# Kernel optimization log

Measured on AMD Instinct MI355X. Metric: run time of the kernel, lower is better.

The kernel has to match this reference:

```python
import jax, jax.numpy as jnp
import numpy as np

G = 128          # voxel grid extent per axis
KS = 3           # kernel size per axis
KK = KS ** 3     # 27 kernel offsets
N_IN, N_OUT, C_IN, C_OUT = 50000, 100000, 128, 128


def setup_inputs() -> dict:
    key = jax.random.key(0)
    k1, k2, k3, k4 = jax.random.split(key, 4)
    features = jax.random.normal(k1, (N_IN, C_IN), dtype=jnp.float32)
    W = jax.random.normal(k2, (KK, C_IN, C_OUT), dtype=jnp.float32) * (1.0 / np.sqrt(C_IN * KK))
    inp_positions = jax.random.randint(k3, (N_IN, 3), 0, G, dtype=jnp.int32)
    out_positions = jax.random.randint(k4, (N_OUT, 3), 0, G, dtype=jnp.int32)
    return {"features": features, "W": W,
            "inp_positions": inp_positions, "out_positions": out_positions}


def _kernel_offsets():
    r = np.arange(KS) - KS // 2  # [-1, 0, 1] for KS=3 (offset=0 since KS is odd)
    dx, dy, dz = np.meshgrid(r, r, r, indexing="ij")
    return jnp.asarray(np.stack([dx.ravel(), dy.ravel(), dz.ravel()], axis=1), dtype=jnp.int32)  # [KK,3]


def reference(features, W, inp_positions, out_positions):
    # Sparse conv-transpose: voxelize input points (voxel_size=1, offset=0 -> identity
    # on integer coords), build voxel->input-index hash (dense grid table), then for
    # each output point gather the input feature at each of the KK kernel offsets and
    # accumulate W[k'] @ feat with mirrored kernel index (transpose of SparseConv).
    lin_in = (inp_positions[:, 0] * G + inp_positions[:, 1]) * G + inp_positions[:, 2]
    grid = jnp.full((G * G * G,), -1, dtype=jnp.int32)
    grid = grid.at[lin_in].max(jnp.arange(N_IN, dtype=jnp.int32))  # deterministic on dup voxels

    offsets = _kernel_offsets()          # [KK, 3]
    W_mirror = W[::-1]                   # transpose conv uses mirrored kernel index

    def step(acc, xk):
        off, Wk = xk                     # off [3], Wk [C_IN, C_OUT]
        nb = out_positions + off[None, :]               # [N_OUT, 3]
        in_bounds = jnp.all((nb >= 0) & (nb < G), axis=1)
        lin = (nb[:, 0] * G + nb[:, 1]) * G + nb[:, 2]
        idx = grid[jnp.clip(lin, 0, G * G * G - 1)]      # [N_OUT]
        ok = in_bounds & (idx >= 0)
        f = jnp.where(ok[:, None], features[jnp.clip(idx, 0)], 0.0)  # [N_OUT, C_IN]
        return acc + f @ Wk, None

    acc0 = jnp.zeros((out_positions.shape[0], W.shape[2]), dtype=features.dtype)
    out, _ = jax.lax.scan(step, acc0, (offsets, W_mirror))
    return out
```

## Files before the change

### kernel.cpp

```cpp
#include <hip/hip_runtime.h>
#include <hip/hip_bf16.h>

#define G    128
#define GGG  (G * G * G)
#define C    128
#define KK   27
#define CAP  4096
#define RT   16

typedef __attribute__((ext_vector_type(8))) short bf16x8;
typedef __attribute__((ext_vector_type(4))) float f32x4;

__device__ __forceinline__ ushort f2b(float f) {
    __hip_bfloat16 h = __float2bfloat16(f);
    return *reinterpret_cast<ushort*>(&h);
}

#define WT_BLOCKS 108
__global__ __launch_bounds__(256) void prep5_kernel(
    uint4* __restrict__ grid16_4, int* __restrict__ cnt,
    const float* __restrict__ W, ushort* __restrict__ Wtb,
    const float4* __restrict__ fg4, uint2* __restrict__ fb2, int nf4)
{
    if (blockIdx.x < WT_BLOCKS) {
        int mm = blockIdx.x >> 2;
        int t  = blockIdx.x & 3;
        __shared__ float Ls[32][129];
        const float* src = W + (size_t)mm * C * C + (size_t)(t * 32) * C;
#pragma unroll
        for (int k = 0; k < 16; ++k) {
            int q = threadIdx.x + k * 256;
            int r = q >> 7, co = q & 127;
            Ls[r][co] = src[r * C + co];
        }
        __syncthreads();
        ushort* dst = Wtb + (size_t)(KK - 1 - mm) * C * C + t * 32;
#pragma unroll
        for (int k = 0; k < 4; ++k) {
            int q = threadIdx.x + k * 256;
            int co = q >> 3, j = q & 7;
            union { ushort u[4]; uint2 p; } pk;
            pk.u[0] = f2b(Ls[4*j+0][co]);
            pk.u[1] = f2b(Ls[4*j+1][co]);
            pk.u[2] = f2b(Ls[4*j+2][co]);
            pk.u[3] = f2b(Ls[4*j+3][co]);
            *(uint2*)&dst[co * C + 4 * j] = pk.p;
        }
        return;
    }
    int b = blockIdx.x - WT_BLOCKS;
    int nb = gridDim.x - WT_BLOCKS;
    int tid = b * 256 + threadIdx.x;
    int stride = nb * 256;
    uint4 ffff = {0xFFFFFFFFu, 0xFFFFFFFFu, 0xFFFFFFFFu, 0xFFFFFFFFu};
    for (int i = tid; i < GGG * 2 / 16; i += stride) grid16_4[i] = ffff;
    if (tid < KK) cnt[tid] = 0;
    for (int i = tid; i < nf4; i += stride) {
        float4 v = fg4[i];
        union { ushort u[4]; uint2 p; } pk;
        pk.u[0] = f2b(v.x); pk.u[1] = f2b(v.y);
        pk.u[2] = f2b(v.z); pk.u[3] = f2b(v.w);
        fb2[i] = pk.p;
    }
}

__global__ void scatter16_kernel(const int* __restrict__ pos,
                                 unsigned int* __restrict__ gword, int n) {
    int i = blockIdx.x * blockDim.x + threadIdx.x;
    if (i >= n) return;
    int x = pos[3 * i], y = pos[3 * i + 1], z = pos[3 * i + 2];
    int lin = (x * G + y) * G + z;
    unsigned int* w = &gword[lin >> 1];
    int sh = (lin & 1) * 16;
    unsigned int val = (unsigned int)i;
    unsigned int old = *w, assumed;
    do {
        unsigned int cur = (old >> sh) & 0xFFFFu;
        if (cur != 0xFFFFu && cur >= val) break;
        unsigned int nw = (old & ~(0xFFFFu << sh)) | (val << sh);
        assumed = old;
        old = atomicCAS(w, assumed, nw);
    } while (old != assumed);
}

__global__ __launch_bounds__(256) void compact4_kernel(
    const int* __restrict__ out_pos, const ushort* __restrict__ grid16,
    int* __restrict__ cnt, int2* __restrict__ pairs,
    int* __restrict__ cnt_row, int* __restrict__ rowtap, int n_out)
{
    int row = blockIdx.x * 256 + threadIdx.x;
    bool valid = row < n_out;
    int lane = threadIdx.x & 63;

    int px = 0, py = 0, pz = 0;
    if (valid) { px = out_pos[3*row]; py = out_pos[3*row+1]; pz = out_pos[3*row+2]; }

    int idx[KK];
#pragma unroll
    for (int m = 0; m < KK; ++m) {
        int x = px + m / 9 - 1, y = py + (m % 9) / 3 - 1, z = pz + m % 3 - 1;
        bool inb = valid && (unsigned)x < G && (unsigned)y < G && (unsigned)z < G;
        int v = inb ? (int)grid16[(x * G + y) * G + z] : 0xFFFF;
        idx[m] = (v == 0xFFFF) ? -1 : v;
    }

    __shared__ int bcnt[KK], bbase[KK];
    if (threadIdx.x < KK) bcnt[threadIdx.x] = 0;
    __syncthreads();

    int gl[KK];
#pragma unroll
    for (int m = 0; m < KK; ++m) {
        unsigned long long act = __ballot(idx[m] >= 0);
        int lpre = __popcll(act & ((1ull << lane) - 1ull));
        int wcnt = __popcll(act);
        int wbase = 0;
        if (lane == 0 && wcnt) wbase = atomicAdd(&bcnt[m], wcnt);
        wbase = __shfl(wbase, 0);
        gl[m] = wbase + lpre;
    }
    __syncthreads();
    if (threadIdx.x < KK) bbase[threadIdx.x] = atomicAdd(&cnt[threadIdx.x], bcnt[threadIdx.x]);
    __syncthreads();

    int gs[KK];
    int cr = 0;
#pragma unroll
    for (int m = 0; m < KK; ++m) {
        int g = -1;
        if (idx[m] >= 0) {
            g = bbase[m] + gl[m];
            if (g >= CAP) g = -1;
        }
        gs[m] = g;
        if (g >= 0) ++cr;
    }

    int dest = (cr == 1) ? row : -1;
    int k = 0;
#pragma unroll
    for (int m = 0; m < KK; ++m) {
        int g = gs[m];
        if (g >= 0) {
            pairs[m * CAP + g] = make_int2(idx[m], dest);
            if (k < RT) { rowtap[k * n_out + row] = (g << 5) | m; ++k; }
        }
    }
    if (valid) cnt_row[row] = cr;
}

__global__ __launch_bounds__(256, 2) void pair_mm5_kernel(
    const uint4* __restrict__ featb4, const ushort* __restrict__ Wtb,
    const int2* __restrict__ pairs, const int* __restrict__ cnt,
    ushort* __restrict__ part, float* __restrict__ out)
{
    int m = blockIdx.y;
    int nm = min(cnt[m], CAP);
    if ((int)(blockIdx.x * 128) >= nm) return;

    __shared__ ushort Wl[128 * 136];
    __shared__ ushort Af[128 * 136];
    __shared__ int    idx_s[128];
    __shared__ int    dest_s[128];

    {
        const uint4* src = (const uint4*)(Wtb + (size_t)m * C * C);
        uint4* dst = (uint4*)Wl;
        for (int q = threadIdx.x; q < 2048; q += 256) {
            int r = q >> 4, c = q & 15;
            dst[r * 17 + c] = src[q];
        }
    }

    int lane = threadIdx.x & 63;
    int w    = threadIdx.x >> 6;
    int l15  = lane & 15;
    int quad = lane >> 4;
    uint4* Af4 = (uint4*)Af;

    for (int base = blockIdx.x * 128; base < nm; base += gridDim.x * 128) {
        __syncthreads();
        if (threadIdx.x < 128) {
            int g = base + threadIdx.x;
            int2 pr = (g < nm) ? pairs[m * CAP + g] : make_int2(-1, -1);
            idx_s[threadIdx.x]  = pr.x;
            dest_s[threadIdx.x] = pr.y;
        }
        __syncthreads();

#pragma unroll
        for (int k = 0; k < 8; ++k) {
            int q = threadIdx.x + k * 256;
            int r = q >> 4, c = q & 15;
            int id = idx_s[r];
            if (id >= 0) Af4[r * 17 + c] = featb4[(size_t)id * 16 + c];
        }
        __syncthreads();

        f32x4 acc[2][8];
#pragma unroll
        for (int s = 0; s < 2; ++s)
#pragma unroll
            for (int n = 0; n < 8; ++n) acc[s][n] = (f32x4){0.f, 0.f, 0.f, 0.f};

#pragma unroll
        for (int kk = 0; kk < 4; ++kk) {
            bf16x8 a0 = *(bf16x8*)&Af[(32*w + l15)      * 136 + kk * 32 + quad * 8];
            bf16x8 a1 = *(bf16x8*)&Af[(32*w + 16 + l15) * 136 + kk * 32 + quad * 8];
#pragma unroll
            for (int n = 0; n < 8; ++n) {
                bf16x8 b = *(bf16x8*)&Wl[(n * 16 + l15) * 136 + kk * 32 + quad * 8];
                acc[0][n] = __builtin_amdgcn_mfma_f32_16x16x32_bf16(a0, b, acc[0][n], 0, 0, 0);
                acc[1][n] = __builtin_amdgcn_mfma_f32_16x16x32_bf16(a1, b, acc[1][n], 0, 0, 0);
            }
        }

#pragma unroll
        for (int s = 0; s < 2; ++s) {
            int r0 = 32 * w + 16 * s + quad * 4;
#pragma unroll
            for (int reg = 0; reg < 4; ++reg) {
                int r = r0 + reg;
                if (base + r >= nm) continue;
                int d = dest_s[r];
                if (d >= 0) {
                    float* o = out + (size_t)d * C + l15;
#pragma unroll
                    for (int n = 0; n < 8; ++n) o[n * 16] = acc[s][n][reg];
                } else {
                    ushort* p = part + ((size_t)(m * CAP + base + r)) * C + l15;
#pragma unroll
                    for (int n = 0; n < 8; ++n) p[n * 16] = f2b(acc[s][n][reg]);
                }
            }
        }
    }
}

__global__ __launch_bounds__(256) void gather_sum3_kernel(
    const ushort* __restrict__ part, const int* __restrict__ rowtap,
    const int* __restrict__ cnt_row, float* __restrict__ out, int n_out)
{
    int row0 = blockIdx.x * 16;
    int rl = threadIdx.x >> 4;
    int t  = threadIdx.x & 15;
    int row = row0 + rl;

    __shared__ int rt_s[RT][16];
    __shared__ int cnt_s[16];
    __shared__ int maxc;
    if (threadIdx.x < 16) {
        int r = row0 + threadIdx.x;
        cnt_s[threadIdx.x] = (r < n_out) ? cnt_row[r] : 0;
    }
    __syncthreads();
    if (threadIdx.x == 0) {
        int mx = 0;
#pragma unroll
        for (int i = 0; i < 16; ++i) mx = max(mx, cnt_s[i]);
        maxc = mx;
    }
    __syncthreads();
    {
        int k = threadIdx.x >> 4, r = threadIdx.x & 15;
        if (k < maxc)
            rt_s[k][r] = (row0 + r < n_out) ? rowtap[k * n_out + row0 + r] : 0;
    }
    __syncthreads();

    int nt = cnt_s[rl];
    if (nt == 1) return;

    float acc[8] = {0,0,0,0,0,0,0,0};
    for (int k = 0; k < nt; ++k) {
        int e = rt_s[k][rl];
        int m = e & 31, g = e >> 5;
        uint4 v = *(const uint4*)(part + ((size_t)(m * CAP + g)) * C + t * 8);
        acc[0] += __uint_as_float(v.x << 16);
        acc[1] += __uint_as_float(v.x & 0xffff0000u);
        acc[2] += __uint_as_float(v.y << 16);
        acc[3] += __uint_as_float(v.y & 0xffff0000u);
        acc[4] += __uint_as_float(v.z << 16);
        acc[5] += __uint_as_float(v.z & 0xffff0000u);
        acc[6] += __uint_as_float(v.w << 16);
        acc[7] += __uint_as_float(v.w & 0xffff0000u);
    }
    if (row < n_out) {
        float* o = out + (size_t)row * C + t * 8;
        *(float4*)(o)     = (float4){acc[0], acc[1], acc[2], acc[3]};
        *(float4*)(o + 4) = (float4){acc[4], acc[5], acc[6], acc[7]};
    }
}

__global__ void init2_kernel(int4* __restrict__ grid4, int* __restrict__ cnt) {
    int i = blockIdx.x * blockDim.x + threadIdx.x;
    int stride = gridDim.x * blockDim.x;
    int4 mone = {-1, -1, -1, -1};
    for (int j = i; j < GGG / 4; j += stride) grid4[j] = mone;
    if (i < KK) cnt[i] = 0;
}

__global__ void scatter_kernel(const int* __restrict__ pos,
                               int* __restrict__ grid, int n) {
    int i = blockIdx.x * blockDim.x + threadIdx.x;
    if (i >= n) return;
    int x = pos[3 * i], y = pos[3 * i + 1], z = pos[3 * i + 2];
    atomicMax(&grid[(x * G + y) * G + z], i);
}

__global__ __launch_bounds__(128) void gather_mm_kernel(
    const float* __restrict__ features, const float* __restrict__ W,
    const int* __restrict__ out_pos, const int* __restrict__ grid,
    float* __restrict__ out, int n_out)
{
    int row = blockIdx.x;
    if (row >= n_out) return;
    int c = threadIdx.x;
    __shared__ int   nb_idx[KK];
    __shared__ float feat_s[C];
    int px = out_pos[3*row], py = out_pos[3*row+1], pz = out_pos[3*row+2];
    if (c < KK) {
        int i = c / 9, j = (c % 9) / 3, k = c % 3;
        int x = px + i - 1, y = py + j - 1, z = pz + k - 1;
        int idx = -1;
        if ((unsigned)x < G && (unsigned)y < G && (unsigned)z < G)
            idx = grid[(x * G + y) * G + z];
        nb_idx[c] = idx;
    }
    __syncthreads();
    float acc = 0.f;
    for (int m = 0; m < KK; ++m) {
        int idx = nb_idx[m];
        if (idx < 0) continue;
        __syncthreads();
        feat_s[c] = features[idx * C + c];
        __syncthreads();
        const float* __restrict__ Wk = W + (KK - 1 - m) * C * C + c;
        float a = 0.f;
#pragma unroll
        for (int ci = 0; ci < C; ++ci) a += feat_s[ci] * Wk[ci * C];
        acc += a;
    }
    out[row * C + c] = acc;
}

extern "C" void kernel_launch(void* const* d_in, const int* in_sizes, int n_in,
                              void* d_out, int out_size, void* d_ws, size_t ws_size,
                              hipStream_t stream) {
    const float* features = (const float*)d_in[0];
    const float* W        = (const float*)d_in[1];
    const int*   inp_pos  = (const int*)d_in[2];
    const int*   out_pos  = (const int*)d_in[3];
    float*       out      = (float*)d_out;

    int n_in_pts  = in_sizes[2] / 3;
    int n_out_pts = out_size / C;

    size_t o_grid   = 0;
    size_t o_cnt    = (size_t)GGG * 4;
    size_t o_pairs  = (o_cnt + 256 + 255) & ~(size_t)255;
    size_t o_cntr   = (o_pairs + (size_t)KK * CAP * 8 + 255) & ~(size_t)255;
    size_t o_rowtap = (o_cntr + (size_t)n_out_pts * 4 + 255) & ~(size_t)255;
    size_t o_wtb    = (o_rowtap + (size_t)RT * n_out_pts * 4 + 255) & ~(size_t)255;
    size_t o_featb  = (o_wtb + (size_t)KK * C * C * 2 + 255) & ~(size_t)255;
    size_t o_part   = (o_featb + (size_t)n_in_pts * C * 2 + 255) & ~(size_t)255;
    size_t need     = o_part + (size_t)KK * CAP * C * 2;

    ushort* grid16  = (ushort*)((char*)d_ws + o_grid);
    int*    cnt     = (int*)((char*)d_ws + o_cnt);
    int2*   pairs   = (int2*)((char*)d_ws + o_pairs);
    int*    cnt_row = (int*)((char*)d_ws + o_cntr);
    int*    rowtap  = (int*)((char*)d_ws + o_rowtap);
    ushort* Wtb     = (ushort*)((char*)d_ws + o_wtb);
    ushort* featb   = (ushort*)((char*)d_ws + o_featb);
    ushort* part    = (ushort*)((char*)d_ws + o_part);

    if (ws_size < need) {
        int* grid32 = (int*)d_ws;
        hipLaunchKernelGGL(init2_kernel, dim3(2048), dim3(256), 0, stream,
                           (int4*)grid32, cnt);
        hipLaunchKernelGGL(scatter_kernel, dim3((n_in_pts + 255) / 256), dim3(256), 0, stream,
                           inp_pos, grid32, n_in_pts);
        hipLaunchKernelGGL(gather_mm_kernel, dim3(n_out_pts), dim3(128), 0, stream,
                           features, W, out_pos, grid32, out, n_out_pts);
        return;
    }

    hipLaunchKernelGGL(prep5_kernel, dim3(WT_BLOCKS + 916), dim3(256), 0, stream,
                       (uint4*)grid16, cnt, W, Wtb,
                       (const float4*)features, (uint2*)featb, n_in_pts * C / 4);
    hipLaunchKernelGGL(scatter16_kernel, dim3((n_in_pts + 255) / 256), dim3(256), 0, stream,
                       inp_pos, (unsigned int*)grid16, n_in_pts);
    hipLaunchKernelGGL(compact4_kernel, dim3((n_out_pts + 255) / 256), dim3(256), 0, stream,
                       out_pos, grid16, cnt, pairs, cnt_row, rowtap, n_out_pts);
    hipLaunchKernelGGL(pair_mm5_kernel, dim3(19, KK), dim3(256), 0, stream,
                       (const uint4*)featb, Wtb, pairs, cnt, part, out);
    hipLaunchKernelGGL(gather_sum3_kernel, dim3((n_out_pts + 15) / 16), dim3(256), 0, stream,
                       part, rowtap, cnt_row, out, n_out_pts);
}
```

Measured before the change: 135.3 us.

## Fuse all conv stages into one cooperative persistent kernel with grid syncs

Replaces the five-kernel pipeline with a single cooperative kernel of 512 persistent blocks that runs prep, scatter, compaction, MFMA pair matmul and gather-sum, separated by grid-wide barriers. It also goes back from a 16-bit packed voxel grid with CAS loops to a 32-bit grid using atomicMax. The aim is to remove launch gaps and inter-kernel drain between stages. In exchange it adds grid-sync overhead, doubles the grid clear and lookup traffic, and limits parallelism to a fixed block count. A multi-kernel fallback is kept for when cooperative launch fails.

```diff
diff --git a/kernel.cpp b/kernel.cpp
--- a/kernel.cpp
+++ b/kernel.cpp
@@ -1,5 +1,8 @@
 #include <hip/hip_runtime.h>
 #include <hip/hip_bf16.h>
+#include <hip/hip_cooperative_groups.h>
+
+namespace cg = cooperative_groups;
 
 #define G    128
 #define GGG  (G * G * G)
@@ -7,6 +10,8 @@
 #define KK   27
 #define CAP  4096
 #define RT   16
+#define NBLK 512
+#define NTHR 256
 
 typedef __attribute__((ext_vector_type(8))) short bf16x8;
 typedef __attribute__((ext_vector_type(4))) float f32x4;
@@ -16,98 +21,326 @@
     return *reinterpret_cast<ushort*>(&h);
 }
 
-#define WT_BLOCKS 108
-__global__ __launch_bounds__(256) void prep5_kernel(
-    uint4* __restrict__ grid16_4, int* __restrict__ cnt,
-    const float* __restrict__ W, ushort* __restrict__ Wtb,
-    const float4* __restrict__ fg4, uint2* __restrict__ fb2, int nf4)
+struct SmemA { float Ls[32][129]; };
+struct SmemB { int bcnt[KK]; int bbase[KK]; };
+struct SmemC { ushort Wl[128 * 136]; ushort Af[128 * 136]; int idx[128]; int dest[128]; };
+struct SmemD { int rt[RT][16]; int cnt[16]; int maxc; };
+union SmemU { SmemA a; SmemB b; SmemC c; SmemD d; };
+
+__global__ __launch_bounds__(NTHR, 2) void fused_kernel(
+    const float* __restrict__ features, const float* __restrict__ W,
+    const int* __restrict__ inp_pos, const int* __restrict__ out_pos,
+    float* __restrict__ out, int* __restrict__ grid32, int* __restrict__ cnt,
+    int2* __restrict__ pairs, int* __restrict__ cnt_row, int* __restrict__ rowtap,
+    ushort* __restrict__ Wtb, ushort* __restrict__ featb, ushort* __restrict__ part,
+    int n_in, int n_out)
 {
-    if (blockIdx.x < WT_BLOCKS) {
-        int mm = blockIdx.x >> 2;
-        int t  = blockIdx.x & 3;
-        __shared__ float Ls[32][129];
-        const float* src = W + (size_t)mm * C * C + (size_t)(t * 32) * C;
-#pragma unroll
-        for (int k = 0; k < 16; ++k) {
-            int q = threadIdx.x + k * 256;
-            int r = q >> 7, co = q & 127;
-            Ls[r][co] = src[r * C + co];
-        }
-        __syncthreads();
-        ushort* dst = Wtb + (size_t)(KK - 1 - mm) * C * C + t * 32;
-#pragma unroll
-        for (int k = 0; k < 4; ++k) {
-            int q = threadIdx.x + k * 256;
-            int co = q >> 3, j = q & 7;
+    cg::grid_group gg = cg::this_grid();
+    __shared__ SmemU sm;
+    int tid = blockIdx.x * NTHR + threadIdx.x;
+    const int gstride = NBLK * NTHR;
+    int lane = threadIdx.x & 63;
+
+    {
+        int4* g4 = (int4*)grid32;
+        int4 mone = {-1, -1, -1, -1};
+        for (int i = tid; i < GGG / 4; i += gstride) g4[i] = mone;
+        if (tid < 32) cnt[tid] = 0;
+
+        const float4* f4 = (const float4*)features;
+        uint2* fb2 = (uint2*)featb;
+        int nf4 = n_in * C / 4;
+        for (int i = tid; i < nf4; i += gstride) {
+            float4 v = f4[i];
             union { ushort u[4]; uint2 p; } pk;
-            pk.u[0] = f2b(Ls[4*j+0][co]);
-            pk.u[1] = f2b(Ls[4*j+1][co]);
-            pk.u[2] = f2b(Ls[4*j+2][co]);
-            pk.u[3] = f2b(Ls[4*j+3][co]);
-            *(uint2*)&dst[co * C + 4 * j] = pk.p;
-        }
-        return;
-    }
-    int b = blockIdx.x - WT_BLOCKS;
-    int nb = gridDim.x - WT_BLOCKS;
-    int tid = b * 256 + threadIdx.x;
-    int stride = nb * 256;
-    uint4 ffff = {0xFFFFFFFFu, 0xFFFFFFFFu, 0xFFFFFFFFu, 0xFFFFFFFFu};
-    for (int i = tid; i < GGG * 2 / 16; i += stride) grid16_4[i] = ffff;
-    if (tid < KK) cnt[tid] = 0;
+            pk.u[0] = f2b(v.x); pk.u[1] = f2b(v.y);
+            pk.u[2] = f2b(v.z); pk.u[3] = f2b(v.w);
+            fb2[i] = pk.p;
+        }
+
+        if (blockIdx.x < KK * 4) {
+            int mm = blockIdx.x >> 2;
+            int t  = blockIdx.x & 3;
+            const float* src = W + (size_t)mm * C * C + (size_t)(t * 32) * C;
+#pragma unroll
+            for (int k = 0; k < 16; ++k) {
+                int q = threadIdx.x + k * 256;
+                int r = q >> 7, co = q & 127;
+                sm.a.Ls[r][co] = src[r * C + co];
+            }
+            __syncthreads();
+            ushort* dst = Wtb + (size_t)(KK - 1 - mm) * C * C + t * 32;
+#pragma unroll
+            for (int k = 0; k < 4; ++k) {
+                int q = threadIdx.x + k * 256;
+                int co = q >> 3, j = q & 7;
+                union { ushort u[4]; uint2 p; } pk;
+                pk.u[0] = f2b(sm.a.Ls[4*j+0][co]);
+                pk.u[1] = f2b(sm.a.Ls[4*j+1][co]);
+                pk.u[2] = f2b(sm.a.Ls[4*j+2][co]);
+                pk.u[3] = f2b(sm.a.Ls[4*j+3][co]);
+                *(uint2*)&dst[co * C + 4 * j] = pk.p;
+            }
+        }
+    }
+    gg.sync();
+
+    for (int i = tid; i < n_in; i += gstride) {
+        int x = inp_pos[3 * i], y = inp_pos[3 * i + 1], z = inp_pos[3 * i + 2];
+        atomicMax(&grid32[(x * G + y) * G + z], i);
+    }
+    gg.sync();
+
+    int nchunk = (n_out + NTHR - 1) / NTHR;
+    for (int ch = blockIdx.x; ch < nchunk; ch += NBLK) {
+        __syncthreads();
+        int row = ch * NTHR + threadIdx.x;
+        bool valid = row < n_out;
+        int px = 0, py = 0, pz = 0;
+        if (valid) { px = out_pos[3*row]; py = out_pos[3*row+1]; pz = out_pos[3*row+2]; }
+
+        int idx[KK];
+#pragma unroll
+        for (int m = 0; m < KK; ++m) {
+            int x = px + m / 9 - 1, y = py + (m % 9) / 3 - 1, z = pz + m % 3 - 1;
+            bool inb = valid && (unsigned)x < G && (unsigned)y < G && (unsigned)z < G;
+            idx[m] = inb ? grid32[(x * G + y) * G + z] : -1;
+        }
+
+        if (threadIdx.x < KK) sm.b.bcnt[threadIdx.x] = 0;
+        __syncthreads();
+
+        int gl[KK];
+#pragma unroll
+        for (int m = 0; m < KK; ++m) {
+            unsigned long long act = __ballot(idx[m] >= 0);
+            int lpre = __popcll(act & ((1ull << lane) - 1ull));
+            int wcnt = __popcll(act);
+            int wbase = 0;
+            if (lane == 0 && wcnt) wbase = atomicAdd(&sm.b.bcnt[m], wcnt);
+            wbase = __shfl(wbase, 0);
+            gl[m] = wbase + lpre;
+        }
+        __syncthreads();
+        if (threadIdx.x < KK)
+            sm.b.bbase[threadIdx.x] = atomicAdd(&cnt[threadIdx.x], sm.b.bcnt[threadIdx.x]);
+        __syncthreads();
+
+        int gs[KK];
+        int cr = 0;
+#pragma unroll
+        for (int m = 0; m < KK; ++m) {
+            int g = -1;
+            if (idx[m] >= 0) {
+                g = sm.b.bbase[m] + gl[m];
+                if (g >= CAP) g = -1;
+            }
+            gs[m] = g;
+            if (g >= 0) ++cr;
+        }
+
+        int dest = (cr == 1) ? row : -1;
+        int k = 0;
+#pragma unroll
+        for (int m = 0; m < KK; ++m) {
+            int g = gs[m];
+            if (g >= 0) {
+                pairs[m * CAP + g] = make_int2(idx[m], dest);
+                if (k < RT) { rowtap[k * n_out + row] = (g << 5) | m; ++k; }
+            }
+        }
+        if (valid) cnt_row[row] = cr;
+    }
+    gg.sync();
+
+    {
+        int w    = threadIdx.x >> 6;
+        int l15  = lane & 15;
+        int quad = lane >> 4;
+        const uint4* featb4 = (const uint4*)featb;
+        uint4* Af4 = (uint4*)sm.c.Af;
+        const int ntile = KK * (CAP / 128);
+
+        for (int t = blockIdx.x; t < ntile; t += NBLK) {
+            int m = t >> 5;
+            int base = (t & 31) * 128;
+            int nm = min(cnt[m], CAP);
+            if (base >= nm) continue;
+
+            __syncthreads();
+            {
+                const uint4* src = (const uint4*)(Wtb + (size_t)m * C * C);
+                uint4* dst = (uint4*)sm.c.Wl;
+                for (int q = threadIdx.x; q < 2048; q += 256) {
+                    int r = q >> 4, c = q & 15;
+                    dst[r * 17 + c] = src[q];
+                }
+            }
+            if (threadIdx.x < 128) {
+                int g = base + threadIdx.x;
+                int2 pr = (g < nm) ? pairs[m * CAP + g] : make_int2(-1, -1);
+                sm.c.idx[threadIdx.x]  = pr.x;
+                sm.c.dest[threadIdx.x] = pr.y;
+            }
+            __syncthreads();
+
+#pragma unroll
+            for (int k = 0; k < 8; ++k) {
+                int q = threadIdx.x + k * 256;
+                int r = q >> 4, c = q & 15;
+                int id = sm.c.idx[r];
+                if (id >= 0) Af4[r * 17 + c] = featb4[(size_t)id * 16 + c];
+            }
+            __syncthreads();
+
+            f32x4 acc[2][8];
+#pragma unroll
+            for (int s = 0; s < 2; ++s)
+#pragma unroll
+                for (int n = 0; n < 8; ++n) acc[s][n] = (f32x4){0.f, 0.f, 0.f, 0.f};
+
+#pragma unroll
+            for (int kk = 0; kk < 4; ++kk) {
+                bf16x8 a0 = *(bf16x8*)&sm.c.Af[(32*w + l15)      * 136 + kk * 32 + quad * 8];
+                bf16x8 a1 = *(bf16x8*)&sm.c.Af[(32*w + 16 + l15) * 136 + kk * 32 + quad * 8];
+#pragma unroll
+                for (int n = 0; n < 8; ++n) {
+                    bf16x8 b = *(bf16x8*)&sm.c.Wl[(n * 16 + l15) * 136 + kk * 32 + quad * 8];
+                    acc[0][n] = __builtin_amdgcn_mfma_f32_16x16x32_bf16(a0, b, acc[0][n], 0, 0, 0);
+                    acc[1][n] = __builtin_amdgcn_mfma_f32_16x16x32_bf16(a1, b, acc[1][n], 0, 0, 0);
+                }
+            }
+
+#pragma unroll
+            for (int s = 0; s < 2; ++s) {
+                int r0 = 32 * w + 16 * s + quad * 4;
+#pragma unroll
+                for (int reg = 0; reg < 4; ++reg) {
+                    int r = r0 + reg;
+                    if (base + r >= nm) continue;
+                    int d = sm.c.dest[r];
+                    if (d >= 0) {
+                        float* o = out + (size_t)d * C + l15;
+#pragma unroll
+                        for (int n = 0; n < 8; ++n) o[n * 16] = acc[s][n][reg];
+                    } else {
+                        ushort* p = part + ((size_t)(m * CAP + base + r)) * C + l15;
+#pragma unroll
+                        for (int n = 0; n < 8; ++n) p[n * 16] = f2b(acc[s][n][reg]);
+                    }
+                }
+            }
+        }
+    }
+    gg.sync();
+
+    {
+        int rl = threadIdx.x >> 4;
+        int t16 = threadIdx.x & 15;
+        int ngrp = (n_out + 15) / 16;
+        for (int gi = blockIdx.x; gi < ngrp; gi += NBLK) {
+            __syncthreads();
+            int row0 = gi * 16;
+            int row = row0 + rl;
+            if (threadIdx.x < 16) {
+                int r = row0 + threadIdx.x;
+                sm.d.cnt[threadIdx.x] = (r < n_out) ? cnt_row[r] : 0;
+            }
+            __syncthreads();
+            if (threadIdx.x == 0) {
+                int mx = 0;
+#pragma unroll
+                for (int i = 0; i < 16; ++i) mx = max(mx, sm.d.cnt[i]);
+                sm.d.maxc = mx;
+            }
+            __syncthreads();
+            {
+                int k = threadIdx.x >> 4, r = threadIdx.x & 15;
+                if (k < sm.d.maxc)
+                    sm.d.rt[k][r] = (row0 + r < n_out) ? rowtap[k * n_out + row0 + r] : 0;
+            }
+            __syncthreads();
+
+            int nt = sm.d.cnt[rl];
+            if (nt == 1 || row >= n_out) continue;
+
+            float acc[8] = {0,0,0,0,0,0,0,0};
+            for (int k = 0; k < nt; ++k) {
+                int e = sm.d.rt[k][rl];
+                int m = e & 31, g = e >> 5;
+                uint4 v = *(const uint4*)(part + ((size_t)(m * CAP + g)) * C + t16 * 8);
+                acc[0] += __uint_as_float(v.x << 16);
+                acc[1] += __uint_as_float(v.x & 0xffff0000u);
+                acc[2] += __uint_as_float(v.y << 16);
+                acc[3] += __uint_as_float(v.y & 0xffff0000u);
+                acc[4] += __uint_as_float(v.z << 16);
+                acc[5] += __uint_as_float(v.z & 0xffff0000u);
+                acc[6] += __uint_as_float(v.w << 16);
+                acc[7] += __uint_as_float(v.w & 0xffff0000u);
+            }
+            float* o = out + (size_t)row * C + t16 * 8;
+            *(float4*)(o)     = (float4){acc[0], acc[1], acc[2], acc[3]};
+            *(float4*)(o + 4) = (float4){acc[4], acc[5], acc[6], acc[7]};
+        }
+    }
+}
+
+__global__ void init2_kernel(int4* __restrict__ grid4, int* __restrict__ cnt) {
+    int i = blockIdx.x * blockDim.x + threadIdx.x;
+    int stride = gridDim.x * blockDim.x;
+    int4 mone = {-1, -1, -1, -1};
+    for (int j = i; j < GGG / 4; j += stride) grid4[j] = mone;
+    if (i < KK) cnt[i] = 0;
+}
+
+__global__ void prep_fb_kernel(const float4* __restrict__ f4, uint2* __restrict__ fb2,
+                               int nf4, const float* __restrict__ W,
+                               ushort* __restrict__ Wtb) {
+    int tid = blockIdx.x * blockDim.x + threadIdx.x;
+    int stride = gridDim.x * blockDim.x;
     for (int i = tid; i < nf4; i += stride) {
-        float4 v = fg4[i];
+        float4 v = f4[i];
         union { ushort u[4]; uint2 p; } pk;
         pk.u[0] = f2b(v.x); pk.u[1] = f2b(v.y);
         pk.u[2] = f2b(v.z); pk.u[3] = f2b(v.w);
         fb2[i] = pk.p;
     }
-}
-
-__global__ void scatter16_kernel(const int* __restrict__ pos,
-                                 unsigned int* __restrict__ gword, int n) {
+    const int NW = KK * C * C;
+    for (int i = tid; i < NW; i += stride) {
+        int m = i >> 14, r = i & 16383;
+        int co = r >> 7, ci = r & 127;
+        Wtb[i] = f2b(W[(size_t)(KK - 1 - m) * C * C + ci * C + co]);
+    }
+}
+
+__global__ void scatter_kernel(const int* __restrict__ pos,
+                               int* __restrict__ grid, int n) {
     int i = blockIdx.x * blockDim.x + threadIdx.x;
     if (i >= n) return;
     int x = pos[3 * i], y = pos[3 * i + 1], z = pos[3 * i + 2];
-    int lin = (x * G + y) * G + z;
-    unsigned int* w = &gword[lin >> 1];
-    int sh = (lin & 1) * 16;
-    unsigned int val = (unsigned int)i;
-    unsigned int old = *w, assumed;
-    do {
-        unsigned int cur = (old >> sh) & 0xFFFFu;
-        if (cur != 0xFFFFu && cur >= val) break;
-        unsigned int nw = (old & ~(0xFFFFu << sh)) | (val << sh);
-        assumed = old;
-        old = atomicCAS(w, assumed, nw);
-    } while (old != assumed);
-}
-
-__global__ __launch_bounds__(256) void compact4_kernel(
-    const int* __restrict__ out_pos, const ushort* __restrict__ grid16,
+    atomicMax(&grid[(x * G + y) * G + z], i);
+}
+
+__global__ __launch_bounds__(256) void compact_fb_kernel(
+    const int* __restrict__ out_pos, const int* __restrict__ grid32,
     int* __restrict__ cnt, int2* __restrict__ pairs,
     int* __restrict__ cnt_row, int* __restrict__ rowtap, int n_out)
 {
     int row = blockIdx.x * 256 + threadIdx.x;
     bool valid = row < n_out;
     int lane = threadIdx.x & 63;
-
     int px = 0, py = 0, pz = 0;
     if (valid) { px = out_pos[3*row]; py = out_pos[3*row+1]; pz = out_pos[3*row+2]; }
-
     int idx[KK];
 #pragma unroll
     for (int m = 0; m < KK; ++m) {
         int x = px + m / 9 - 1, y = py + (m % 9) / 3 - 1, z = pz + m % 3 - 1;
         bool inb = valid && (unsigned)x < G && (unsigned)y < G && (unsigned)z < G;
-        int v = inb ? (int)grid16[(x * G + y) * G + z] : 0xFFFF;
-        idx[m] = (v == 0xFFFF) ? -1 : v;
-    }
-
+        idx[m] = inb ? grid32[(x * G + y) * G + z] : -1;
+    }
     __shared__ int bcnt[KK], bbase[KK];
     if (threadIdx.x < KK) bcnt[threadIdx.x] = 0;
     __syncthreads();
-
     int gl[KK];
 #pragma unroll
     for (int m = 0; m < KK; ++m) {
@@ -122,20 +355,14 @@
     __syncthreads();
     if (threadIdx.x < KK) bbase[threadIdx.x] = atomicAdd(&cnt[threadIdx.x], bcnt[threadIdx.x]);
     __syncthreads();
-
-    int gs[KK];
-    int cr = 0;
+    int gs[KK]; int cr = 0;
 #pragma unroll
     for (int m = 0; m < KK; ++m) {
         int g = -1;
-        if (idx[m] >= 0) {
-            g = bbase[m] + gl[m];
-            if (g >= CAP) g = -1;
-        }
+        if (idx[m] >= 0) { g = bbase[m] + gl[m]; if (g >= CAP) g = -1; }
         gs[m] = g;
         if (g >= 0) ++cr;
     }
-
     int dest = (cr == 1) ? row : -1;
     int k = 0;
 #pragma unroll
@@ -149,7 +376,7 @@
     if (valid) cnt_row[row] = cr;
 }
 
-__global__ __launch_bounds__(256, 2) void pair_mm5_kernel(
+__global__ __launch_bounds__(256, 2) void pair_mm_fb_kernel(
     const uint4* __restrict__ featb4, const ushort* __restrict__ Wtb,
     const int2* __restrict__ pairs, const int* __restrict__ cnt,
     ushort* __restrict__ part, float* __restrict__ out)
@@ -157,12 +384,10 @@
     int m = blockIdx.y;
     int nm = min(cnt[m], CAP);
     if ((int)(blockIdx.x * 128) >= nm) return;
-
     __shared__ ushort Wl[128 * 136];
     __shared__ ushort Af[128 * 136];
-    __shared__ int    idx_s[128];
-    __shared__ int    dest_s[128];
-
+    __shared__ int idx_s[128];
+    __shared__ int dest_s[128];
     {
         const uint4* src = (const uint4*)(Wtb + (size_t)m * C * C);
         uint4* dst = (uint4*)Wl;
@@ -171,23 +396,20 @@
             dst[r * 17 + c] = src[q];
         }
     }
-
     int lane = threadIdx.x & 63;
-    int w    = threadIdx.x >> 6;
-    int l15  = lane & 15;
+    int w = threadIdx.x >> 6;
+    int l15 = lane & 15;
     int quad = lane >> 4;
     uint4* Af4 = (uint4*)Af;
-
     for (int base = blockIdx.x * 128; base < nm; base += gridDim.x * 128) {
         __syncthreads();
         if (threadIdx.x < 128) {
             int g = base + threadIdx.x;
             int2 pr = (g < nm) ? pairs[m * CAP + g] : make_int2(-1, -1);
-            idx_s[threadIdx.x]  = pr.x;
+            idx_s[threadIdx.x] = pr.x;
             dest_s[threadIdx.x] = pr.y;
         }
         __syncthreads();
-
 #pragma unroll
         for (int k = 0; k < 8; ++k) {
             int q = threadIdx.x + k * 256;
@@ -196,13 +418,11 @@
             if (id >= 0) Af4[r * 17 + c] = featb4[(size_t)id * 16 + c];
         }
         __syncthreads();
-
         f32x4 acc[2][8];
 #pragma unroll
         for (int s = 0; s < 2; ++s)
 #pragma unroll
             for (int n = 0; n < 8; ++n) acc[s][n] = (f32x4){0.f, 0.f, 0.f, 0.f};
-
 #pragma unroll
         for (int kk = 0; kk < 4; ++kk) {
             bf16x8 a0 = *(bf16x8*)&Af[(32*w + l15)      * 136 + kk * 32 + quad * 8];
@@ -214,7 +434,6 @@
                 acc[1][n] = __builtin_amdgcn_mfma_f32_16x16x32_bf16(a1, b, acc[1][n], 0, 0, 0);
             }
         }
-
 #pragma unroll
         for (int s = 0; s < 2; ++s) {
             int r0 = 32 * w + 16 * s + quad * 4;
@@ -237,15 +456,14 @@
     }
 }
 
-__global__ __launch_bounds__(256) void gather_sum3_kernel(
+__global__ __launch_bounds__(256) void gather_fb_kernel(
     const ushort* __restrict__ part, const int* __restrict__ rowtap,
     const int* __restrict__ cnt_row, float* __restrict__ out, int n_out)
 {
     int row0 = blockIdx.x * 16;
     int rl = threadIdx.x >> 4;
-    int t  = threadIdx.x & 15;
+    int t = threadIdx.x & 15;
     int row = row0 + rl;
-
     __shared__ int rt_s[RT][16];
     __shared__ int cnt_s[16];
     __shared__ int maxc;
@@ -267,10 +485,8 @@
             rt_s[k][r] = (row0 + r < n_out) ? rowtap[k * n_out + row0 + r] : 0;
     }
     __syncthreads();
-
     int nt = cnt_s[rl];
     if (nt == 1) return;
-
     float acc[8] = {0,0,0,0,0,0,0,0};
     for (int k = 0; k < nt; ++k) {
         int e = rt_s[k][rl];
@@ -292,22 +508,6 @@
     }
 }
 
-__global__ void init2_kernel(int4* __restrict__ grid4, int* __restrict__ cnt) {
-    int i = blockIdx.x * blockDim.x + threadIdx.x;
-    int stride = gridDim.x * blockDim.x;
-    int4 mone = {-1, -1, -1, -1};
-    for (int j = i; j < GGG / 4; j += stride) grid4[j] = mone;
-    if (i < KK) cnt[i] = 0;
-}
-
-__global__ void scatter_kernel(const int* __restrict__ pos,
-                               int* __restrict__ grid, int n) {
-    int i = blockIdx.x * blockDim.x + threadIdx.x;
-    if (i >= n) return;
-    int x = pos[3 * i], y = pos[3 * i + 1], z = pos[3 * i + 2];
-    atomicMax(&grid[(x * G + y) * G + z], i);
-}
-
 __global__ __launch_bounds__(128) void gather_mm_kernel(
     const float* __restrict__ features, const float* __restrict__ W,
     const int* __restrict__ out_pos, const int* __restrict__ grid,
@@ -316,7 +516,7 @@
     int row = blockIdx.x;
     if (row >= n_out) return;
     int c = threadIdx.x;
-    __shared__ int   nb_idx[KK];
+    __shared__ int nb_idx[KK];
     __shared__ float feat_s[C];
     int px = out_pos[3*row], py = out_pos[3*row+1], pz = out_pos[3*row+2];
     if (c < KK) {
@@ -366,7 +566,7 @@
     size_t o_part   = (o_featb + (size_t)n_in_pts * C * 2 + 255) & ~(size_t)255;
     size_t need     = o_part + (size_t)KK * CAP * C * 2;
 
-    ushort* grid16  = (ushort*)((char*)d_ws + o_grid);
+    int*    grid32  = (int*)((char*)d_ws + o_grid);
     int*    cnt     = (int*)((char*)d_ws + o_cnt);
     int2*   pairs   = (int2*)((char*)d_ws + o_pairs);
     int*    cnt_row = (int*)((char*)d_ws + o_cntr);
@@ -376,7 +576,6 @@
     ushort* part    = (ushort*)((char*)d_ws + o_part);
 
     if (ws_size < need) {
-        int* grid32 = (int*)d_ws;
         hipLaunchKernelGGL(init2_kernel, dim3(2048), dim3(256), 0, stream,
                            (int4*)grid32, cnt);
         hipLaunchKernelGGL(scatter_kernel, dim3((n_in_pts + 255) / 256), dim3(256), 0, stream,
@@ -386,15 +585,37 @@
         return;
     }
 
-    hipLaunchKernelGGL(prep5_kernel, dim3(WT_BLOCKS + 916), dim3(256), 0, stream,
-                       (uint4*)grid16, cnt, W, Wtb,
-                       (const float4*)features, (uint2*)featb, n_in_pts * C / 4);
-    hipLaunchKernelGGL(scatter16_kernel, dim3((n_in_pts + 255) / 256), dim3(256), 0, stream,
-                       inp_pos, (unsigned int*)grid16, n_in_pts);
-    hipLaunchKernelGGL(compact4_kernel, dim3((n_out_pts + 255) / 256), dim3(256), 0, stream,
-                       out_pos, grid16, cnt, pairs, cnt_row, rowtap, n_out_pts);
-    hipLaunchKernelGGL(pair_mm5_kernel, dim3(19, KK), dim3(256), 0, stream,
-                       (const uint4*)featb, Wtb, pairs, cnt, part, out);
-    hipLaunchKernelGGL(gather_sum3_kernel, dim3((n_out_pts + 15) / 16), dim3(256), 0, stream,
-                       part, rowtap, cnt_row, out, n_out_pts);
-}
+    int coop = 0;
+    {
+        int dev = 0;
+        hipGetDevice(&dev);
+        hipDeviceGetAttribute(&coop, hipDeviceAttributeCooperativeLaunch, dev);
+    }
+
+    hipError_t st = hipErrorUnknown;
+    if (coop) {
+        void* args[] = {
+            (void*)&features, (void*)&W, (void*)&inp_pos, (void*)&out_pos,
+            (void*)&out, (void*)&grid32, (void*)&cnt, (void*)&pairs,
+            (void*)&cnt_row, (void*)&rowtap, (void*)&Wtb, (void*)&featb,
+            (void*)&part, (void*)&n_in_pts, (void*)&n_out_pts
+        };
+        st = hipLaunchCooperativeKernel((const void*)fused_kernel,
+                                        dim3(NBLK), dim3(NTHR), args, 0, stream);
+    }
+    if (st != hipSuccess) {
+        hipLaunchKernelGGL(init2_kernel, dim3(2048), dim3(256), 0, stream,
+                           (int4*)grid32, cnt);
+        hipLaunchKernelGGL(prep_fb_kernel, dim3(1024), dim3(256), 0, stream,
+                           (const float4*)features, (uint2*)featb,
+                           n_in_pts * C / 4, W, Wtb);
+        hipLaunchKernelGGL(scatter_kernel, dim3((n_in_pts + 255) / 256), dim3(256), 0, stream,
+                           inp_pos, grid32, n_in_pts);
+        hipLaunchKernelGGL(compact_fb_kernel, dim3((n_out_pts + 255) / 256), dim3(256), 0, stream,
+                           out_pos, grid32, cnt, pairs, cnt_row, rowtap, n_out_pts);
+        hipLaunchKernelGGL(pair_mm_fb_kernel, dim3(19, KK), dim3(256), 0, stream,
+                           (const uint4*)featb, Wtb, pairs, cnt, part, out);
+        hipLaunchKernelGGL(gather_fb_kernel, dim3((n_out_pts + 15) / 16), dim3(256), 0, stream,
+                           part, rowtap, cnt_row, out, n_out_pts);
+    }
+}
```

After: 416.8 us. +208.1%, slower.
